# Kernel tuning notes

Measured on AMD Instinct MI355X. Metric: run time of the kernel, lower is better.

## Reference

```python
import jax, jax.numpy as jnp
import numpy as np

# Config (matches init_kwargs)
N_PARTS = 4
N_DATASETS = 2
N_VOLUMES = 16
N_TRANSFORMS = 2
TEMP_FAC = 0.1
BS = N_PARTS * N_DATASETS * N_VOLUMES          # 128
N_TOTAL = BS * (N_TRANSFORMS + 1)              # 384 rows in reg_pred
D_FEAT = 131072
PD = N_PARTS * N_DATASETS                      # class period for denominator exclusion
EPS = 1e-6


def setup_inputs() -> dict:
    key = jax.random.key(0)
    reg_pred = jax.random.normal(key, (N_TOTAL, D_FEAT), dtype=jnp.float32)
    return {"reg_pred": reg_pred}


def reference(reg_pred) -> jnp.ndarray:
    # Cosine similarity with torch's eps clamp on each norm.
    norms = jnp.maximum(jnp.linalg.norm(reg_pred, axis=1, keepdims=True), EPS)
    xn = reg_pred / norms                                   # [N, D]
    sims = (xn @ xn.T) / TEMP_FAC                           # [N, N] full cos-sim matrix
    e = jnp.exp(sims)

    # Denominator for pos_index p excludes every column j with j % PD == p % PD
    # (dataset_similar=False, within_dataset=False). Precompute per-class column sums.
    jmod = jnp.arange(N_TOTAL) % PD                          # [N]
    class_sum = jax.ops.segment_sum(e.T, jmod, num_segments=PD).T  # [N, PD]
    row_sum = jnp.sum(e, axis=1)                             # [N]

    p = jnp.arange(BS)
    rem = p % PD
    i1 = p
    i2 = BS + p
    i3 = (p + PD) % N_TOTAL
    i4 = (BS + p + PD) % N_TOTAL
    i5 = 2 * BS + p
    i6 = (2 * BS + p + PD) % N_TOTAL

    def pair_loss(a, b):
        en = e[a, b]                                         # exp(cos(xi,xj)/t), [BS]
        den_a = row_sum[a] - class_sum[a, rem]               # sum exp over den indexes
        den_b = row_sum[b] - class_sum[b, rem]
        return jnp.sum(-jnp.log(en / (en + den_a)) - jnp.log(en / (en + den_b)))

    total = (pair_loss(i1, i2) + pair_loss(i3, i4) + pair_loss(i1, i3)
             + pair_loss(i2, i4) + pair_loss(i5, i6) + pair_loss(i2, i5)
             + pair_loss(i4, i6))
    return total / (N_TRANSFORMS * 3 * BS)
```

## Files before the change

kernel.cpp:

```cpp
#include <hip/hip_runtime.h>
#include <hip/hip_bf16.h>

#define N_TOTAL 384
#define BS 128
#define PD 8
#define D_FEAT 131072
#define EPS 1e-6f

#define NSTRIP 256
#define COLS_PER (D_FEAT / NSTRIP)
#define CHUNK 32
#define NCH (COLS_PER / CHUNK)
#define NSLOT 24

typedef __attribute__((ext_vector_type(4))) float f32x4;
typedef __attribute__((ext_vector_type(8))) __bf16 bf16x8;
typedef __attribute__((ext_vector_type(4))) __bf16 bf16x4;

typedef __attribute__((address_space(1))) const unsigned int gu32;
typedef __attribute__((address_space(3))) unsigned int lu32;

__device__ __forceinline__ void gload16(const void* g, void* l) {
    __builtin_amdgcn_global_load_lds((gu32*)g, (lu32*)l, 16, 0, 0);
}

static __device__ const int SAt[8][3] = {{0,0,0},{0,0,0},{1,1,1},{1,1,1},
                                         {2,2,4},{2,2,4},{3,3,5},{3,3,5}};
static __device__ const int SBt[8][3] = {{0,1,2},{3,4,5},{0,1,2},{3,4,5},
                                         {2,3,4},{4,5,5},{2,3,4},{4,5,5}};
static __device__ const int SRB2[NSLOT] = {0,0,0, 0,0,0, 1,1,1, 1,1,1,
                                           2,2,4, 2,2,4, 3,3,5, 3,3,5};
static __device__ const int SCB2[NSLOT] = {0,1,2, 3,4,5, 0,1,2, 3,4,5,
                                           2,3,4, 4,5,5, 2,3,4, 4,5,5};

__device__ __forceinline__ float gsym(const float* __restrict__ G, int i, int j) {
    return ((i >> 7) <= (j >> 7)) ? G[(size_t)i * N_TOTAL + j]
                                  : G[(size_t)j * N_TOTAL + i];
}

__device__ __forceinline__ bf16x8 fragld(const char* bptr, int row, int kg) {
    const int k = row & 7;
    const f32x4 lo = *(const f32x4*)(bptr + row * 128 + (((2 * kg)     ^ k) * 16));
    const f32x4 hi = *(const f32x4*)(bptr + row * 128 + (((2 * kg + 1) ^ k) * 16));
    bf16x8 r;
    r[0] = (__bf16)lo[0]; r[1] = (__bf16)lo[1]; r[2] = (__bf16)lo[2]; r[3] = (__bf16)lo[3];
    r[4] = (__bf16)hi[0]; r[5] = (__bf16)hi[1]; r[6] = (__bf16)hi[2]; r[7] = (__bf16)hi[3];
    return r;
}

__global__ __launch_bounds__(512) void gram_fused_kernel(const float* __restrict__ X,
                                                         __bf16* __restrict__ P) {
    __shared__ char sm[2][N_TOTAL * 128];

    const int strip = blockIdx.x;
    const int tid  = threadIdx.x;
    const int wave = tid >> 6;
    const int lane = tid & 63;
    const int r16  = lane & 15;
    const int kg   = lane >> 4;

    const int A0 = SAt[wave][0] * 64, A2 = SAt[wave][2] * 64;
    const int B0 = SBt[wave][0] * 64, B1 = SBt[wave][1] * 64, B2 = SBt[wave][2] * 64;

    const int lg = (tid & 7) ^ ((tid >> 3) & 7);
    const char* src0 = (const char*)(X + (size_t)(tid >> 3) * D_FEAT
                                       + (size_t)strip * COLS_PER) + lg * 16;

    f32x4 acc0[4][4], acc1[4][4], acc2[4][4];
#pragma unroll
    for (int m = 0; m < 4; m++)
#pragma unroll
        for (int n = 0; n < 4; n++) {
            acc0[m][n] = (f32x4)(0.0f); acc1[m][n] = (f32x4)(0.0f); acc2[m][n] = (f32x4)(0.0f);
        }

#define STAGE(buf, t)                                                                     \
    _Pragma("unroll") for (int s = 0; s < 6; s++)                                         \
        gload16(src0 + (size_t)s * (64ull * D_FEAT * 4) + (size_t)(t) * 128,              \
                (char*)sm[buf] + s * 8192 + tid * 16);

#define SUBT(accX, Bb)                                                                    \
    do {                                                                                  \
        bf16x8 bf[4];                                                                     \
        _Pragma("unroll") for (int n = 0; n < 4; n++)                                     \
            bf[n] = fragld(bptr, (Bb) + n * 16 + r16, kg);                                \
        _Pragma("unroll") for (int m = 0; m < 4; m++)                                     \
            _Pragma("unroll") for (int n = 0; n < 4; n++)                                 \
                accX[m][n] = __builtin_amdgcn_mfma_f32_16x16x32_bf16(af[m], bf[n],        \
                                                                     accX[m][n], 0, 0, 0);\
    } while (0)

    STAGE(0, 0);
    __syncthreads();

    for (int t = 0; t < NCH; ++t) {
        const int b = t & 1;
        if (t + 1 < NCH) STAGE(b ^ 1, t + 1);
        const char* bptr = sm[b];
        bf16x8 af[4];
#pragma unroll
        for (int m = 0; m < 4; m++) af[m] = fragld(bptr, A0 + m * 16 + r16, kg);
        SUBT(acc0, B0);
        SUBT(acc1, B1);
#pragma unroll
        for (int m = 0; m < 4; m++) af[m] = fragld(bptr, A2 + m * 16 + r16, kg);
        SUBT(acc2, B2);
        __syncthreads();
    }
#undef STAGE
#undef SUBT

    const int crow = (lane >> 4) * 4;
    const int ccol = lane & 15;
#define STOREP(accX, s)                                                                   \
    do {                                                                                  \
        __bf16* base = P + ((size_t)strip * NSLOT + wave * 3 + (s)) * 4096;               \
        _Pragma("unroll") for (int m = 0; m < 4; m++)                                     \
            _Pragma("unroll") for (int n = 0; n < 4; n++) {                               \
                bf16x4 v;                                                                 \
                v[0] = (__bf16)accX[m][n][0]; v[1] = (__bf16)accX[m][n][1];               \
                v[2] = (__bf16)accX[m][n][2]; v[3] = (__bf16)accX[m][n][3];               \
                *(bf16x4*)(base + (n * 16 + ccol) * 64 + m * 16 + crow) = v;              \
            }                                                                             \
    } while (0)
    STOREP(acc0, 0);
    STOREP(acc1, 1);
    STOREP(acc2, 2);
#undef STOREP
}

__global__ __launch_bounds__(256) void reduce_kernel(const __bf16* __restrict__ P,
                                                     float* __restrict__ G) {
    const int b     = blockIdx.x;
    const int chunk = b & 15;
    const int slot  = b >> 4;
    const int e     = chunk * 256 + threadIdx.x;

    const __bf16* p = P + (size_t)slot * 4096 + e;
    float s = 0.0f;
#pragma unroll 16
    for (int strip = 0; strip < NSTRIP; ++strip)
        s += (float)p[(size_t)strip * NSLOT * 4096];

    const int rb  = SRB2[slot] * 64;
    const int cb  = SCB2[slot] * 64;
    const int col = e >> 6;
    const int row = e & 63;
    G[(size_t)(rb + row) * N_TOTAL + cb + col] = s;
}

__global__ __launch_bounds__(128) void den_kernel(const float* __restrict__ G,
                                                  float* __restrict__ den) {
    const int i = blockIdx.x;
    __shared__ float sInv[N_TOTAL];
    for (int j = threadIdx.x; j < N_TOTAL; j += 128) {
        const float n = sqrtf(G[(size_t)j * N_TOTAL + j]);
        sInv[j] = 1.0f / fmaxf(n, EPS);
    }
    __syncthreads();

    const float mi  = sInv[i] * 10.0f;
    const int   myc = i & 7;
    float s = 0.0f;
    for (int j = threadIdx.x; j < N_TOTAL; j += 128) {
        if ((j & 7) != myc)
            s += expf(gsym(G, i, j) * mi * sInv[j]);
    }
#pragma unroll
    for (int off = 32; off > 0; off >>= 1) s += __shfl_down(s, off, 64);
    __shared__ float partial[2];
    if ((threadIdx.x & 63) == 0) partial[threadIdx.x >> 6] = s;
    __syncthreads();
    if (threadIdx.x == 0) den[i] = partial[0] + partial[1];
}

__global__ __launch_bounds__(256) void loss_kernel(const float* __restrict__ G,
                                                   const float* __restrict__ den,
                                                   float* __restrict__ out) {
    __shared__ float sInv[N_TOTAL];
    for (int j = threadIdx.x; j < N_TOTAL; j += 256) {
        const float n = sqrtf(G[(size_t)j * N_TOTAL + j]);
        sInv[j] = 1.0f / fmaxf(n, EPS);
    }
    __syncthreads();

    float s = 0.0f;
    for (int idx = threadIdx.x; idx < 7 * BS; idx += 256) {
        const int p   = idx & (BS - 1);
        const int set = idx >> 7;
        int a, b;
        switch (set) {
            case 0:  a = p;                        b = BS + p;                      break;
            case 1:  a = (p + PD) % N_TOTAL;       b = (BS + p + PD) % N_TOTAL;     break;
            case 2:  a = p;                        b = (p + PD) % N_TOTAL;          break;
            case 3:  a = BS + p;                   b = (BS + p + PD) % N_TOTAL;     break;
            case 4:  a = 2 * BS + p;               b = (2 * BS + p + PD) % N_TOTAL; break;
            case 5:  a = BS + p;                   b = 2 * BS + p;                  break;
            default: a = (BS + p + PD) % N_TOTAL;  b = (2 * BS + p + PD) % N_TOTAL; break;
        }
        const float en = expf(gsym(G, a, b) * sInv[a] * sInv[b] * 10.0f);
        s += log1pf(den[a] / en) + log1pf(den[b] / en);
    }
#pragma unroll
    for (int off = 32; off > 0; off >>= 1) s += __shfl_down(s, off, 64);
    __shared__ float partial[4];
    if ((threadIdx.x & 63) == 0) partial[threadIdx.x >> 6] = s;
    __syncthreads();
    if (threadIdx.x == 0)
        out[0] = (partial[0] + partial[1] + partial[2] + partial[3]) / 768.0f;
}

extern "C" void kernel_launch(void* const* d_in, const int* in_sizes, int n_in,
                              void* d_out, int out_size, void* d_ws, size_t ws_size,
                              hipStream_t stream) {
    (void)in_sizes; (void)n_in; (void)out_size; (void)ws_size;
    const float* X   = (const float*)d_in[0];
    float*       out = (float*)d_out;
    float*       G   = (float*)d_ws;
    float*       den = G + (size_t)N_TOTAL * N_TOTAL;
    __bf16*      P   = (__bf16*)((char*)d_ws + (1u << 20));

    gram_fused_kernel<<<NSTRIP, 512, 0, stream>>>(X, P);
    reduce_kernel<<<NSLOT * 16, 256, 0, stream>>>(P, G);
    den_kernel<<<N_TOTAL, 128, 0, stream>>>(G, den);
    loss_kernel<<<1, 256, 0, stream>>>(G, den, out);
}
```

Before: 72.75 us.

## Triple-buffer Gram staging with vmcnt waits and vectorize partial reduce

The Gram kernel moves from double to triple LDS buffering, so loads run two chunks ahead. Each iteration now uses an explicit vmcnt wait and a single barrier instead of two __syncthreads, keeping more global-to-LDS traffic in flight during the MFMA work. The reduce kernel reads two bf16 partials per 32-bit load, converts them with bit shifts, and writes two G entries per thread, halving its thread count. LDS use grows to 144KB per block, which may affect occupancy and relies on correct vmcnt accounting of the global_load_lds ops.

```diff
diff --git a/kernel.cpp b/kernel.cpp
--- a/kernel.cpp
+++ b/kernel.cpp
@@ -50,7 +50,7 @@
 
 __global__ __launch_bounds__(512) void gram_fused_kernel(const float* __restrict__ X,
                                                          __bf16* __restrict__ P) {
-    __shared__ char sm[2][N_TOTAL * 128];
+    __shared__ char sm[3][N_TOTAL * 128];
 
     const int strip = blockIdx.x;
     const int tid  = threadIdx.x;
@@ -91,12 +91,16 @@
     } while (0)
 
     STAGE(0, 0);
-    __syncthreads();
+    STAGE(1, 1);
 
     for (int t = 0; t < NCH; ++t) {
-        const int b = t & 1;
-        if (t + 1 < NCH) STAGE(b ^ 1, t + 1);
-        const char* bptr = sm[b];
+        if (t < NCH - 1) asm volatile("s_waitcnt vmcnt(6)" ::: "memory");
+        else             asm volatile("s_waitcnt vmcnt(0)" ::: "memory");
+        __builtin_amdgcn_sched_barrier(0);
+        __builtin_amdgcn_s_barrier();
+        if (t + 2 < NCH) STAGE((t + 2) % 3, t + 2);
+
+        const char* bptr = sm[t % 3];
         bf16x8 af[4];
 #pragma unroll
         for (int m = 0; m < 4; m++) af[m] = fragld(bptr, A0 + m * 16 + r16, kg);
@@ -105,7 +109,6 @@
 #pragma unroll
         for (int m = 0; m < 4; m++) af[m] = fragld(bptr, A2 + m * 16 + r16, kg);
         SUBT(acc2, B2);
-        __syncthreads();
     }
 #undef STAGE
 #undef SUBT
@@ -129,24 +132,28 @@
 #undef STOREP
 }
 
-__global__ __launch_bounds__(256) void reduce_kernel(const __bf16* __restrict__ P,
+__global__ __launch_bounds__(128) void reduce_kernel(const __bf16* __restrict__ P,
                                                      float* __restrict__ G) {
-    const int b     = blockIdx.x;
-    const int chunk = b & 15;
-    const int slot  = b >> 4;
-    const int e     = chunk * 256 + threadIdx.x;
-
-    const __bf16* p = P + (size_t)slot * 4096 + e;
-    float s = 0.0f;
+    const int gidx = blockIdx.x * 128 + threadIdx.x;
+    const int slot = gidx >> 11;
+    const int pe   = (gidx & 2047) * 2;
+
+    const unsigned* p = (const unsigned*)(P + (size_t)slot * 4096 + pe);
+    const size_t stride = (size_t)NSLOT * 4096 / 2;
+    float s0 = 0.0f, s1 = 0.0f;
 #pragma unroll 16
-    for (int strip = 0; strip < NSTRIP; ++strip)
-        s += (float)p[(size_t)strip * NSLOT * 4096];
+    for (int strip = 0; strip < NSTRIP; ++strip) {
+        const unsigned u = p[stride * strip];
+        s0 += __uint_as_float(u << 16);
+        s1 += __uint_as_float(u & 0xffff0000u);
+    }
 
     const int rb  = SRB2[slot] * 64;
     const int cb  = SCB2[slot] * 64;
-    const int col = e >> 6;
-    const int row = e & 63;
-    G[(size_t)(rb + row) * N_TOTAL + cb + col] = s;
+    const int col = pe >> 6;
+    const int row = pe & 63;
+    G[(size_t)(rb + row)     * N_TOTAL + cb + col] = s0;
+    G[(size_t)(rb + row + 1) * N_TOTAL + cb + col] = s1;
 }
 
 __global__ __launch_bounds__(128) void den_kernel(const float* __restrict__ G,
@@ -221,7 +228,7 @@
     __bf16*      P   = (__bf16*)((char*)d_ws + (1u << 20));
 
     gram_fused_kernel<<<NSTRIP, 512, 0, stream>>>(X, P);
-    reduce_kernel<<<NSLOT * 16, 256, 0, stream>>>(P, G);
+    reduce_kernel<<<384, 128, 0, stream>>>(P, G);
     den_kernel<<<N_TOTAL, 128, 0, stream>>>(G, den);
     loss_kernel<<<1, 256, 0, stream>>>(G, den, out);
 }
```

Result: no change. 73.89 us (+1.6%).
